# Kernel tuning notes

Hardware: AMD Instinct MI355X
Metric: run time of the kernel (lower is better)

The kernel has to match this reference:

```python
import jax, jax.numpy as jnp
import numpy as np
from itertools import product

N = 200000      # occupied fine voxels
G = 256         # grid extent per axis
C0, C1 = 32, 64 # nPlanes
EPS = 1e-4      # BatchNormBlock eps


def _enc(p):
    return (p[:, 0].astype(np.int64) * G + p[:, 1]) * G + p[:, 2]


def _lookup(q, keys):
    # keys: sorted encoded positions; returns index into position array, sentinel=len(keys) if absent
    n = keys.shape[0]
    valid = ((q >= 0) & (q < G)).all(1)
    qe = _enc(np.clip(q, 0, G - 1))
    i = np.searchsorted(keys, qe)
    ic = np.clip(i, 0, n - 1)
    found = valid & (keys[ic] == qe)
    return np.where(found, ic, n).astype(np.int32)


def _build_geometry():
    rng = np.random.default_rng(0)
    lin = np.sort(rng.choice(G ** 3, size=N, replace=False))
    pos = np.stack(np.unravel_index(lin, (G, G, G)), -1).astype(np.int64)  # [N,3], enc(pos)==lin sorted
    keys = lin
    off27 = np.array(list(product((-1, 0, 1), repeat=3)), dtype=np.int64)
    nbr_fine = np.stack([_lookup(pos + o, keys) for o in off27])  # [27,N]
    # Convolution.calculate_grid: even positions among pos+{-1,0}^3, min>=0, unique, then /2
    f8 = np.array(list(product((-1, 0), repeat=3)), dtype=np.int64)
    cand = (pos[:, None, :] + f8[None]).reshape(-1, 3)
    cand = cand[cand.min(1) >= 0]
    cand = cand[(cand % 2 == 0).all(1)]
    cand = np.unique(cand, axis=0)
    cpos = cand // 2                       # [M,3] coarse coords
    ckeys = _enc(cpos)                     # lexsorted rows -> sorted keys
    off2 = np.array([[(i >> 2) & 1, (i >> 1) & 1, i & 1] for i in range(8)], dtype=np.int64)
    down_idx = np.stack([_lookup(2 * cpos + o, keys) for o in off2])  # [8,M] into fine feats

    def _lookup_c(q):
        n = ckeys.shape[0]
        valid = ((q >= 0) & (q < G)).all(1)
        qe = _enc(np.clip(q, 0, G - 1))
        i = np.searchsorted(ckeys, qe)
        ic = np.clip(i, 0, n - 1)
        found = valid & (ckeys[ic] == qe)
        return np.where(found, ic, n).astype(np.int32)

    nbr_coarse = np.stack([_lookup_c(cpos + o) for o in off27])  # [27,M]
    up_cidx = _lookup_c(pos // 2)  # [N], always found (coverage guaranteed by calculate_grid)
    up_k = ((pos[:, 0] % 2) * 4 + (pos[:, 1] % 2) * 2 + (pos[:, 2] % 2)).astype(np.int32)
    return nbr_fine, nbr_coarse, down_idx, up_cidx, up_k


def setup_inputs() -> dict:
    nbr_fine, nbr_coarse, down_idx, up_cidx, up_k = _build_geometry()
    key = jax.random.key(0)
    ks = jax.random.split(key, 8)

    def w(k, shape, fan_in):
        return jax.random.normal(k, shape, jnp.float32) * (1.0 / np.sqrt(fan_in))

    return dict(
        feat=jax.random.normal(ks[0], (N, C0), jnp.float32),
        w_sub1=w(ks[1], (27, C0, C0), 27 * C0),
        w_down=w(ks[2], (8, C0, C1), 8 * C0),
        w_sub2=w(ks[3], (27, C1, C1), 27 * C1),
        w_up=w(ks[4], (8, C1, C0), 8 * C1),
        w_sub3=w(ks[5], (27, 2 * C0, C0), 27 * 2 * C0),
        g1=jnp.ones(C0), b1=jnp.zeros(C0),
        g2=jnp.ones(C0), b2=jnp.zeros(C0),
        g3=jnp.ones(C1), b3=jnp.zeros(C1),
        g4=jnp.ones(C1), b4=jnp.zeros(C1),
        g5=jnp.ones(2 * C0), b5=jnp.zeros(2 * C0),
        nbr_fine=jnp.asarray(nbr_fine), nbr_coarse=jnp.asarray(nbr_coarse),
        down_idx=jnp.asarray(down_idx), up_cidx=jnp.asarray(up_cidx),
        up_k=jnp.asarray(up_k),
    )


def _bn_relu(x, g, b):
    # BatchNormBlock (training-mode batch stats over concatenated voxels) + ReLUBlock
    mu = x.mean(0)
    var = x.var(0)
    return jax.nn.relu(g * (x - mu) * jax.lax.rsqrt(var + EPS) + b)


def _sparse_conv(feat, nbr, W):
    # gather-GEMM-accumulate: feat [P,Cin], nbr [K,M] (sentinel P -> zero), W [K,Cin,Cout]
    fpad = jnp.concatenate([feat, jnp.zeros((1, feat.shape[1]), feat.dtype)], 0)

    def body(acc, kw):
        idx, w = kw
        return acc + fpad[idx] @ w, None

    acc0 = jnp.zeros((nbr.shape[1], W.shape[2]), feat.dtype)
    out, _ = jax.lax.scan(body, acc0, (nbr, W))
    return out


def _sparse_deconv(cfeat, up_cidx, up_k, W):
    # stride-2 transpose conv: each fine voxel reads its unique coarse parent with kernel tap up_k
    g = cfeat[up_cidx]  # [N,Cin]
    out = jnp.zeros((g.shape[0], W.shape[2]), cfeat.dtype)
    for k in range(8):
        out = out + jnp.where(up_k == k, 1.0, 0.0)[:, None] * (g @ W[k])
    return out


def reference(feat, w_sub1, w_down, w_sub2, w_up, w_sub3,
              g1, b1, g2, b2, g3, b3, g4, b4, g5, b5,
              nbr_fine, nbr_coarse, down_idx, up_cidx, up_k):
    # block(32->32): BN -> ReLU -> SubmanifoldSparseConv 3x3x3
    x = _sparse_conv(_bn_relu(feat, g1, b1), nbr_fine, w_sub1)
    skip = x  # ConcatFeat
    # BN -> ReLU -> Convolution 2x2x2 (downsample 32->64)
    xc = _sparse_conv(_bn_relu(x, g2, b2), down_idx, w_down)
    # inner level block(64->64)
    xc = _sparse_conv(_bn_relu(xc, g3, b3), nbr_coarse, w_sub2)
    # BN -> ReLU -> DeConvolution 2x2x2 (upsample 64->32)
    xf = _sparse_deconv(_bn_relu(xc, g4, b4), up_cidx, up_k, w_up)
    # JoinFeat: concat(skip, upsampled)
    x = jnp.concatenate([skip, xf], -1)
    # block(64->32)
    x = _sparse_conv(_bn_relu(x, g5, b5), nbr_fine, w_sub3)
    return x
```

## Files before the change

### kernel.cpp

```cpp
#include <hip/hip_runtime.h>


#define EPS 1e-4f

typedef __attribute__((ext_vector_type(8))) short short8;
typedef __attribute__((ext_vector_type(4))) float f32x4;

__device__ __forceinline__ unsigned short f2bf(float f) {
    union { float f; unsigned int u; } v; v.f = f;
    unsigned int r = v.u + 0x7fffu + ((v.u >> 16) & 1u);
    return (unsigned short)(r >> 16);
}

__global__ void zero_kernel(float* p, long n) {
    long i = (long)blockIdx.x * 256 + threadIdx.x;
    if (i < n) p[i] = 0.f;
}

template <int C>
__global__ __launch_bounds__(256) void bn_stats(const float* __restrict__ x,
                                                int rows, int stride,
                                                float* __restrict__ stats) {
    const int tid = threadIdx.x;
    const int c = tid & (C - 1);
    const int g = tid / C;
    const int GR = 256 / C;
    float s = 0.f, s2 = 0.f;
    for (int r = blockIdx.x * GR + g; r < rows; r += gridDim.x * GR) {
        float v = x[(size_t)r * stride + c];
        s += v; s2 += v * v;
    }
    __shared__ float sh[2][256];
    sh[0][tid] = s; sh[1][tid] = s2;
    __syncthreads();
    for (int off = 128; off >= C; off >>= 1) {
        if (tid < off) { sh[0][tid] += sh[0][tid + off]; sh[1][tid] += sh[1][tid + off]; }
        __syncthreads();
    }
    if (tid < C) {
        atomicAdd(&stats[c], sh[0][tid]);
        atomicAdd(&stats[C + c], sh[1][tid]);
    }
}

template <int C, int CSPLIT>
__global__ __launch_bounds__(256) void bn_norm_relu_bf16(
    const float* __restrict__ x, int rows, int stride,
    const float* __restrict__ stA, const float* __restrict__ stB,
    const float* __restrict__ gamma, const float* __restrict__ beta,
    unsigned short* __restrict__ y) {
    constexpr int TPR = C / 8;
    int gid = blockIdx.x * 256 + threadIdx.x;
    int r = gid / TPR, t = gid % TPR;
    if (r > rows) return;
    short8 o8;
    if (r == rows) {
        for (int j = 0; j < 8; ++j) o8[j] = 0;
    } else {
        const float inv_n = 1.0f / (float)rows;
        const float* xr = x + (size_t)r * stride + t * 8;
        float4 v0 = *(const float4*)(xr);
        float4 v1 = *(const float4*)(xr + 4);
        float vv[8] = {v0.x, v0.y, v0.z, v0.w, v1.x, v1.y, v1.z, v1.w};
#pragma unroll
        for (int j = 0; j < 8; ++j) {
            int c = t * 8 + j;
            const float* st = (c < CSPLIT) ? stA : stB;
            int cc = (c < CSPLIT) ? c : c - CSPLIT;
            int cs = (c < CSPLIT) ? CSPLIT : (C - CSPLIT);
            float mu = st[cc] * inv_n;
            float var = st[cs + cc] * inv_n - mu * mu;
            float sc = gamma[c] * rsqrtf(var + EPS);
            float shf = beta[c] - mu * sc;
            float ov = fmaxf(0.f, fmaf(vv[j], sc, shf));
            o8[j] = (short)f2bf(ov);
        }
    }
    *(short8*)(y + (size_t)r * C + t * 8) = o8;
}

__device__ __forceinline__ void wt_seg(const float* W, unsigned short* WT,
                                       int id, int CIN, int COUT) {
    int r = id % (CIN * COUT);
    int t = id / (CIN * COUT);
    int co = r / CIN;
    int ci = r % CIN;
    int ksub = CIN >> 5;
    int nt = co >> 4, l15 = co & 15;
    int kf = (ksub > 1) ? (ci >> 5) : 0;
    int qq = (ci >> 3) & 3;
    int e  = ci & 7;
    int off = ((nt * ksub + kf) * 64 + (qq * 16 + l15)) * 8 + e;
    WT[(size_t)t * CIN * COUT + off] = f2bf(W[(size_t)t * CIN * COUT + ci * COUT + co]);
}
__global__ __launch_bounds__(256) void wt_transpose_all(
    const float* w1, const float* wd, const float* w2, const float* w3,
    const float* wu, unsigned short* o1, unsigned short* od,
    unsigned short* o2, unsigned short* o3, unsigned short* ou) {
    int id = blockIdx.x * 256 + threadIdx.x;
    if (id < 27648) { wt_seg(w1, o1, id, 32, 32); return; }
    id -= 27648;
    if (id < 16384) { wt_seg(wd, od, id, 32, 64); return; }
    id -= 16384;
    if (id < 110592) { wt_seg(w2, o2, id, 64, 64); return; }
    id -= 110592;
    if (id < 55296) { wt_seg(w3, o3, id, 64, 32); return; }
    id -= 55296;
    if (id < 16384) { wt_seg(wu, ou, id, 64, 32); return; }
}

__global__ __launch_bounds__(256) void build_rb_up(
    const int* __restrict__ up_cidx, const int* __restrict__ up_k,
    int rows, int cap, int2* __restrict__ rb, int* __restrict__ cnt) {
    const int s = blockIdx.y;
    const int lane = threadIdx.x & 63;
    const int wave = threadIdx.x >> 6;
    const long wbase = (long)blockIdx.x * 1024 + wave * 256;

    unsigned long long masks[4];
    int cs[4], ok[4], tot[4], wtotal = 0;
#pragma unroll
    for (int c = 0; c < 4; ++c) {
        long i = wbase + c * 64 + lane;
        int seg = (i < rows) ? up_k[i] : -1;
        cs[c] = (i < rows) ? up_cidx[i] : 0;
        ok[c] = (seg == s);
        masks[c] = __ballot(ok[c]);
        tot[c] = __popcll(masks[c]);
        wtotal += tot[c];
    }
    __shared__ int sh[5];
    if (lane == 0) sh[wave] = wtotal;
    __syncthreads();
    if (threadIdx.x == 0) {
        int t = sh[0] + sh[1] + sh[2] + sh[3];
        sh[4] = t ? atomicAdd(&cnt[s * 32], t) : 0;
    }
    __syncthreads();
    int base = sh[4];
    for (int w = 0; w < wave; ++w) base += sh[w];
#pragma unroll
    for (int c = 0; c < 4; ++c) {
        if (ok[c]) {
            int rank = __popcll(masks[c] & ((1ull << lane) - 1ull));
            int j = base + rank;
            if (j < cap)
                rb[(size_t)s * cap + j] = make_int2((int)(wbase + c * 64 + lane), cs[c]);
        }
        base += tot[c];
    }
}


template <int CIN, int COT, int NTAP, int MT>
__global__ __launch_bounds__(256) void conv_dense(
    const unsigned short* __restrict__ fpad,
    const int* __restrict__ nbr,
    const unsigned short* __restrict__ WT,
    float* __restrict__ out,
    float* __restrict__ stats,
    int rows, int P, int out_stride) {
    constexpr int N_SUB = COT / 16;
    constexpr int K_SUB = CIN / 32;
    constexpr int TAP_SH = COT * CIN;
    constexpr int TOT_I = TAP_SH / 512;
    __shared__ unsigned short ldsB[2][TAP_SH];
    const int tid = threadIdx.x;
    const int wave = tid >> 6;
    const int lane = tid & 63;
    const int q = lane >> 4;
    const int l15 = lane & 15;
    const int m0 = blockIdx.x * (64 * MT) + wave * (16 * MT);

    int mrow[MT], mok[MT];
#pragma unroll
    for (int mt = 0; mt < MT; ++mt) {
        int m = m0 + mt * 16 + l15;
        mok[mt] = (m < rows);
        mrow[mt] = mok[mt] ? m : 0;
    }

    f32x4 acc[MT][N_SUB];
#pragma unroll
    for (int mt = 0; mt < MT; ++mt)
#pragma unroll
        for (int nt = 0; nt < N_SUB; ++nt) acc[mt][nt] = (f32x4){0.f, 0.f, 0.f, 0.f};

    short8 aA[MT][K_SUB], aB[MT][K_SUB];
    short8 b[N_SUB][K_SUB];
    int idxC[MT];

    auto stage_b = [&](int k, int buf) {
        const unsigned short* src = WT + (size_t)k * TAP_SH;
        for (int j = wave; j < TOT_I; j += 4) {
            __builtin_amdgcn_global_load_lds(
                (const __attribute__((address_space(1))) void*)(src + j * 512 + lane * 8),
                (__attribute__((address_space(3))) void*)(&ldsB[buf][j * 512]),
                16, 0, 0);
        }
    };
    auto load_b_lds = [&](int buf) {
#pragma unroll
        for (int nt = 0; nt < N_SUB; ++nt)
#pragma unroll
            for (int kf = 0; kf < K_SUB; ++kf)
                b[nt][kf] = *(const short8*)(&ldsB[buf][((nt * K_SUB + kf) * 64 + lane) * 8]);
    };
    auto load_idx = [&](int k) {
#pragma unroll
        for (int mt = 0; mt < MT; ++mt)
            idxC[mt] = mok[mt] ? nbr[(size_t)k * rows + mrow[mt]] : P;
    };
    auto gather = [&](short8 (&a)[MT][K_SUB]) {
#pragma unroll
        for (int mt = 0; mt < MT; ++mt) {
            const unsigned short* ap = fpad + (size_t)idxC[mt] * CIN + q * 8;
#pragma unroll
            for (int kf = 0; kf < K_SUB; ++kf)
                a[mt][kf] = *(const short8*)(ap + kf * 32);
        }
    };
    auto do_mfma = [&](short8 (&a)[MT][K_SUB]) {
#pragma unroll
        for (int mt = 0; mt < MT; ++mt)
#pragma unroll
            for (int nt = 0; nt < N_SUB; ++nt)
#pragma unroll
                for (int kf = 0; kf < K_SUB; ++kf)
                    acc[mt][nt] = __builtin_amdgcn_mfma_f32_16x16x32_bf16(
                        a[mt][kf], b[nt][kf], acc[mt][nt], 0, 0, 0);
    };

    stage_b(0, 0);
    load_idx(0);
    gather(aA);
    if (NTAP > 1) load_idx(1);
    __syncthreads();

#pragma unroll
    for (int k = 0; k < NTAP; ++k) {
        const int cur = k & 1;
        load_b_lds(cur);
        if (k + 1 < NTAP) {
            stage_b(k + 1, cur ^ 1);
            if (k & 1) gather(aA); else gather(aB);
            if (k + 2 < NTAP) load_idx(k + 2);
        }
        if (k & 1) do_mfma(aB); else do_mfma(aA);
        if (k + 1 < NTAP) __syncthreads();
    }

#pragma unroll
    for (int mt = 0; mt < MT; ++mt)
#pragma unroll
        for (int i = 0; i < 4; ++i) {
            int row = m0 + mt * 16 + q * 4 + i;
            if (row < rows) {
#pragma unroll
                for (int nt = 0; nt < N_SUB; ++nt)
                    out[(size_t)row * out_stride + nt * 16 + l15] = acc[mt][nt][i];
            }
        }

    if (stats) {
        __shared__ float ssum[COT], ssq[COT];
        for (int i = tid; i < 2 * COT; i += 256)
            (i < COT ? ssum[i] : ssq[i - COT]) = 0.f;
        __syncthreads();
#pragma unroll
        for (int nt = 0; nt < N_SUB; ++nt) {
            float s = 0.f, s2 = 0.f;
#pragma unroll
            for (int mt = 0; mt < MT; ++mt)
#pragma unroll
                for (int i = 0; i < 4; ++i) {
                    float v = acc[mt][nt][i];
                    s += v; s2 += v * v;
                }
            s += __shfl_xor(s, 16);  s += __shfl_xor(s, 32);
            s2 += __shfl_xor(s2, 16); s2 += __shfl_xor(s2, 32);
            if (q == 0) {
                atomicAdd(&ssum[nt * 16 + l15], s);
                atomicAdd(&ssq[nt * 16 + l15], s2);
            }
        }
        __syncthreads();
        if (tid < COT) {
            atomicAdd(&stats[tid], ssum[tid]);
            atomicAdd(&stats[COT + tid], ssq[tid]);
        }
    }
}

template <int CIN, int COT, bool ATOMIC>
__global__ __launch_bounds__(256) void conv_sparse(
    const unsigned short* __restrict__ fpad,
    const int2* __restrict__ rb,
    const int* __restrict__ cnt,
    const unsigned short* __restrict__ WT,
    float* __restrict__ out,
    float* __restrict__ stats,
    int cap, int kskip, int P, int out_stride) {
    constexpr int N_SUB = COT / 16;
    constexpr int K_SUB = CIN / 32;
    const int tap = blockIdx.y;
    int n = cnt[tap * 32];
    n = n < cap ? n : cap;
    const int nbx = gridDim.x;
    const int step = (nbx >> 3) | 1;
    const int px = (int)((blockIdx.x + (unsigned)tap * step) % (unsigned)nbx);
    const int base0 = px * 128;
    if (base0 >= n) return;
    const int k = tap + (tap >= kskip ? 1 : 0);
    const int tid = threadIdx.x;
    const int wave = tid >> 6;
    const int lane = tid & 63;
    const int q = lane >> 4;
    const int l15 = lane & 15;
    const int base = base0 + wave * 32;
    const int2* seg = rb + (size_t)tap * cap;

    f32x4 acc[2][N_SUB];
#pragma unroll
    for (int mt = 0; mt < 2; ++mt)
#pragma unroll
        for (int nt = 0; nt < N_SUB; ++nt) acc[mt][nt] = (f32x4){0.f, 0.f, 0.f, 0.f};

    short8 a[2][K_SUB], b[N_SUB][K_SUB];
#pragma unroll
    for (int mt = 0; mt < 2; ++mt) {
        int j = base + mt * 16 + l15;
        int src = (j < n) ? seg[j].y : P;
#pragma unroll
        for (int kf = 0; kf < K_SUB; ++kf)
            a[mt][kf] = *(const short8*)(fpad + (size_t)src * CIN + kf * 32 + q * 8);
    }
    const unsigned short* Wk = WT + (size_t)k * COT * CIN;
#pragma unroll
    for (int nt = 0; nt < N_SUB; ++nt)
#pragma unroll
        for (int kf = 0; kf < K_SUB; ++kf)
            b[nt][kf] = *(const short8*)(Wk + ((nt * K_SUB + kf) * 64 + lane) * 8);
#pragma unroll
    for (int mt = 0; mt < 2; ++mt)
#pragma unroll
        for (int nt = 0; nt < N_SUB; ++nt)
#pragma unroll
            for (int kf = 0; kf < K_SUB; ++kf)
                acc[mt][nt] = __builtin_amdgcn_mfma_f32_16x16x32_bf16(
                    a[mt][kf], b[nt][kf], acc[mt][nt], 0, 0, 0);

#pragma unroll
    for (int mt = 0; mt < 2; ++mt)
#pragma unroll
        for (int i = 0; i < 4; ++i) {
            int j = base + mt * 16 + q * 4 + i;
            if (j < n) {
                int row = seg[j].x;
                float* o = out + (size_t)row * out_stride + l15;
#pragma unroll
                for (int nt = 0; nt < N_SUB; ++nt) {
                    if (ATOMIC) atomicAdd(o + nt * 16, acc[mt][nt][i]);
                    else        o[nt * 16] = acc[mt][nt][i];
                }
            }
        }

    if (!ATOMIC && stats) {
        __shared__ float ssum[COT], ssq[COT];
        for (int i = tid; i < 2 * COT; i += 256)
            (i < COT ? ssum[i] : ssq[i - COT]) = 0.f;
        __syncthreads();
#pragma unroll
        for (int nt = 0; nt < N_SUB; ++nt) {
            float s = 0.f, s2 = 0.f;
#pragma unroll
            for (int mt = 0; mt < 2; ++mt)
#pragma unroll
                for (int i = 0; i < 4; ++i) {
                    float v = acc[mt][nt][i];
                    s += v; s2 += v * v;
                }
            s += __shfl_xor(s, 16);  s += __shfl_xor(s, 32);
            s2 += __shfl_xor(s2, 16); s2 += __shfl_xor(s2, 32);
            if (q == 0) {
                atomicAdd(&ssum[nt * 16 + l15], s);
                atomicAdd(&ssq[nt * 16 + l15], s2);
            }
        }
        __syncthreads();
        if (tid < COT) {
            atomicAdd(&stats[tid], ssum[tid]);
            atomicAdd(&stats[COT + tid], ssq[tid]);
        }
    }
}

static inline int ceil_div(long a, long b) { return (int)((a + b - 1) / b); }

extern "C" void kernel_launch(void* const* d_in, const int* in_sizes, int n_in,
                              void* d_out, int out_size, void* d_ws, size_t ws_size,
                              hipStream_t stream) {
    const float* feat   = (const float*)d_in[0];
    const float* w_sub1 = (const float*)d_in[1];
    const float* w_down = (const float*)d_in[2];
    const float* w_sub2 = (const float*)d_in[3];
    const float* w_up   = (const float*)d_in[4];
    const float* w_sub3 = (const float*)d_in[5];
    const float* g1 = (const float*)d_in[6],  *b1 = (const float*)d_in[7];
    const float* g2 = (const float*)d_in[8],  *b2 = (const float*)d_in[9];
    const float* g3 = (const float*)d_in[10], *b3 = (const float*)d_in[11];
    const float* g4 = (const float*)d_in[12], *b4 = (const float*)d_in[13];
    const float* g5 = (const float*)d_in[14], *b5 = (const float*)d_in[15];
    const int* nbr_fine   = (const int*)d_in[16];
    const int* nbr_coarse = (const int*)d_in[17];
    const int* down_idx   = (const int*)d_in[18];
    const int* up_cidx    = (const int*)d_in[19];
    const int* up_k       = (const int*)d_in[20];

    const int N = in_sizes[0] / 32;
    const int M = in_sizes[17] / 27;
    const size_t maxr = (size_t)((N > M ? N : M) + 1);

    const int cap_u = 32768;

    char* ws = (char*)d_ws;
    size_t off = 0;
    auto alloc = [&](size_t bytes) { void* p = ws + off; off += (bytes + 255) & ~(size_t)255; return p; };
    float* stats = (float*)alloc(768 * sizeof(float));
    int*   cnts  = (int*)alloc(1024 * sizeof(int));
    const size_t zero_words = off / 4;
    float* D  = (float*)alloc((size_t)N * 64 * sizeof(float));
    float* Cf = (float*)alloc((size_t)M * 64 * sizeof(float));
    unsigned short* FA = (unsigned short*)alloc(maxr * 64 * 2);
    unsigned short* FB = (unsigned short*)alloc(maxr * 64 * 2);
    int2* rb_up = (int2*)alloc((size_t)8 * cap_u * sizeof(int2));
    unsigned short* w1t = (unsigned short*)alloc(27 * 32 * 32 * 2);
    unsigned short* wdt = (unsigned short*)alloc(8 * 32 * 64 * 2);
    unsigned short* w2t = (unsigned short*)alloc(27 * 64 * 64 * 2);
    unsigned short* w3t = (unsigned short*)alloc(27 * 64 * 32 * 2);
    unsigned short* wupT = (unsigned short*)alloc(8 * 64 * 32 * 2);

    float* st0 = stats + 0 * 128;
    float* st1 = stats + 1 * 128;
    float* st2 = stats + 2 * 128;
    float* st3 = stats + 3 * 128;
    float* st4 = stats + 4 * 128;
    int* cnt_up = cnts;

    zero_kernel<<<ceil_div((long)zero_words, 256), 256, 0, stream>>>(stats, (long)zero_words);
    wt_transpose_all<<<ceil_div(226304, 256), 256, 0, stream>>>(
        w_sub1, w_down, w_sub2, w_sub3, w_up, w1t, wdt, w2t, w3t, wupT);
    build_rb_up<<<dim3(ceil_div(N, 1024), 8), 256, 0, stream>>>(
        up_cidx, up_k, N, cap_u, rb_up, cnt_up);

    bn_stats<32><<<256, 256, 0, stream>>>(feat, N, 32, st0);
    bn_norm_relu_bf16<32, 32><<<ceil_div((long)(N + 1) * 4, 256), 256, 0, stream>>>(
        feat, N, 32, st0, st0, g1, b1, FA);
    conv_dense<32, 32, 27, 2><<<ceil_div(N, 128), 256, 0, stream>>>(
        FA, nbr_fine, w1t, D, st1, N, N, 64);
    bn_norm_relu_bf16<32, 32><<<ceil_div((long)(N + 1) * 4, 256), 256, 0, stream>>>(
        D, N, 64, st1, st1, g2, b2, FB);
    conv_dense<32, 64, 8, 2><<<ceil_div(M, 128), 256, 0, stream>>>(
        FB, down_idx, wdt, Cf, st2, M, N, 64);
    bn_norm_relu_bf16<64, 64><<<ceil_div((long)(M + 1) * 8, 256), 256, 0, stream>>>(
        Cf, M, 64, st2, st2, g3, b3, FA);
    conv_dense<64, 64, 27, 2><<<ceil_div(M, 128), 256, 0, stream>>>(
        FA, nbr_coarse, w2t, Cf, st3, M, M, 64);
    bn_norm_relu_bf16<64, 64><<<ceil_div((long)(M + 1) * 8, 256), 256, 0, stream>>>(
        Cf, M, 64, st3, st3, g4, b4, FB);
    conv_sparse<64, 32, false><<<dim3(cap_u / 128, 8), 256, 0, stream>>>(
        FB, rb_up, cnt_up, wupT, D + 32, st4, cap_u, 99, M, 64);
    bn_norm_relu_bf16<64, 32><<<ceil_div((long)(N + 1) * 8, 256), 256, 0, stream>>>(
        D, N, 64, st1, st4, g5, b5, FA);
    conv_dense<64, 32, 27, 2><<<ceil_div(N, 128), 256, 0, stream>>>(
        FA, nbr_fine, w3t, (float*)d_out, nullptr, N, N, 32);
}
```

Measured before the change: 540.9 us.

## Stage multiple weight taps per phase to cut block barriers in dense conv

Groups TPP kernel taps into each LDS staging phase of the gather-MFMA conv, double-buffering whole phases instead of single taps. A __syncthreads is now needed only at phase boundaries rather than after every tap, and weight prefetch is issued once per phase. In exchange, LDS usage per block grows several-fold, which may lower occupancy. Per-layer TPP values are chosen for each conv.

```diff
diff --git a/kernel.cpp b/kernel.cpp
--- a/kernel.cpp
+++ b/kernel.cpp
@@ -152,7 +152,7 @@
 }
 
 
-template <int CIN, int COT, int NTAP, int MT>
+template <int CIN, int COT, int NTAP, int MT, int TPP>
 __global__ __launch_bounds__(256) void conv_dense(
     const unsigned short* __restrict__ fpad,
     const int* __restrict__ nbr,
@@ -163,8 +163,9 @@
     constexpr int N_SUB = COT / 16;
     constexpr int K_SUB = CIN / 32;
     constexpr int TAP_SH = COT * CIN;
-    constexpr int TOT_I = TAP_SH / 512;
-    __shared__ unsigned short ldsB[2][TAP_SH];
+    constexpr int PHASES = (NTAP + TPP - 1) / TPP;
+    constexpr int NBUF = (PHASES > 1) ? 2 : 1;
+    __shared__ unsigned short ldsB[NBUF][TPP * TAP_SH];
     const int tid = threadIdx.x;
     const int wave = tid >> 6;
     const int lane = tid & 63;
@@ -190,21 +191,25 @@
     short8 b[N_SUB][K_SUB];
     int idxC[MT];
 
-    auto stage_b = [&](int k, int buf) {
-        const unsigned short* src = WT + (size_t)k * TAP_SH;
-        for (int j = wave; j < TOT_I; j += 4) {
+    auto stage_phase = [&](int ph, int buf) {
+        const int t0 = ph * TPP;
+        const int cnt = (t0 + TPP <= NTAP) ? TPP : (NTAP - t0);
+        const unsigned short* src = WT + (size_t)t0 * TAP_SH;
+        const int tot = cnt * TAP_SH / 512;
+        for (int j = wave; j < tot; j += 4) {
             __builtin_amdgcn_global_load_lds(
                 (const __attribute__((address_space(1))) void*)(src + j * 512 + lane * 8),
                 (__attribute__((address_space(3))) void*)(&ldsB[buf][j * 512]),
                 16, 0, 0);
         }
     };
-    auto load_b_lds = [&](int buf) {
+    auto load_b_lds = [&](int buf, int kk) {
 #pragma unroll
         for (int nt = 0; nt < N_SUB; ++nt)
 #pragma unroll
             for (int kf = 0; kf < K_SUB; ++kf)
-                b[nt][kf] = *(const short8*)(&ldsB[buf][((nt * K_SUB + kf) * 64 + lane) * 8]);
+                b[nt][kf] = *(const short8*)(
+                    &ldsB[buf][kk * TAP_SH + ((nt * K_SUB + kf) * 64 + lane) * 8]);
     };
     auto load_idx = [&](int k) {
 #pragma unroll
@@ -231,7 +236,7 @@
                         a[mt][kf], b[nt][kf], acc[mt][nt], 0, 0, 0);
     };
 
-    stage_b(0, 0);
+    stage_phase(0, 0);
     load_idx(0);
     gather(aA);
     if (NTAP > 1) load_idx(1);
@@ -239,15 +244,19 @@
 
 #pragma unroll
     for (int k = 0; k < NTAP; ++k) {
-        const int cur = k & 1;
-        load_b_lds(cur);
+        constexpr int NB1 = NBUF - 1;
+        const int ph = k / TPP;
+        const int cur = ph & NB1;
+        load_b_lds(cur, k - ph * TPP);
+        if (k % TPP == 0 && ph + 1 < PHASES)
+            stage_phase(ph + 1, (ph + 1) & NB1);
         if (k + 1 < NTAP) {
-            stage_b(k + 1, cur ^ 1);
             if (k & 1) gather(aA); else gather(aB);
             if (k + 2 < NTAP) load_idx(k + 2);
         }
         if (k & 1) do_mfma(aB); else do_mfma(aA);
-        if (k + 1 < NTAP) __syncthreads();
+        if ((k + 1) % TPP == 0 && (k + 1) < NTAP)
+            __syncthreads();
     }
 
 #pragma unroll
@@ -457,15 +466,15 @@
     bn_stats<32><<<256, 256, 0, stream>>>(feat, N, 32, st0);
     bn_norm_relu_bf16<32, 32><<<ceil_div((long)(N + 1) * 4, 256), 256, 0, stream>>>(
         feat, N, 32, st0, st0, g1, b1, FA);
-    conv_dense<32, 32, 27, 2><<<ceil_div(N, 128), 256, 0, stream>>>(
+    conv_dense<32, 32, 27, 2, 9><<<ceil_div(N, 128), 256, 0, stream>>>(
         FA, nbr_fine, w1t, D, st1, N, N, 64);
     bn_norm_relu_bf16<32, 32><<<ceil_div((long)(N + 1) * 4, 256), 256, 0, stream>>>(
         D, N, 64, st1, st1, g2, b2, FB);
-    conv_dense<32, 64, 8, 2><<<ceil_div(M, 128), 256, 0, stream>>>(
+    conv_dense<32, 64, 8, 2, 8><<<ceil_div(M, 128), 256, 0, stream>>>(
         FB, down_idx, wdt, Cf, st2, M, N, 64);
     bn_norm_relu_bf16<64, 64><<<ceil_div((long)(M + 1) * 8, 256), 256, 0, stream>>>(
         Cf, M, 64, st2, st2, g3, b3, FA);
-    conv_dense<64, 64, 27, 2><<<ceil_div(M, 128), 256, 0, stream>>>(
+    conv_dense<64, 64, 27, 2, 3><<<ceil_div(M, 128), 256, 0, stream>>>(
         FA, nbr_coarse, w2t, Cf, st3, M, M, 64);
     bn_norm_relu_bf16<64, 64><<<ceil_div((long)(M + 1) * 8, 256), 256, 0, stream>>>(
         Cf, M, 64, st3, st3, g4, b4, FB);
@@ -473,6 +482,6 @@
         FB, rb_up, cnt_up, wupT, D + 32, st4, cap_u, 99, M, 64);
     bn_norm_relu_bf16<64, 32><<<ceil_div((long)(N + 1) * 8, 256), 256, 0, stream>>>(
         D, N, 64, st1, st4, g5, b5, FA);
-    conv_dense<64, 32, 27, 2><<<ceil_div(N, 128), 256, 0, stream>>>(
+    conv_dense<64, 32, 27, 2, 5><<<ceil_div(N, 128), 256, 0, stream>>>(
         FA, nbr_fine, w3t, (float*)d_out, nullptr, N, N, 32);
 }
```

Measured after the change: 540.4 us. No clear change (-0.1%).
